# Performance work log

Measured on AMD Instinct MI355X. Metric: run time of the kernel, lower is better.

Reference implementation:

```python
import jax, jax.numpy as jnp
import numpy as np

BLOCK_LEN = 128
NUM_HEADS = 16


def setup_inputs() -> dict:
    key = jax.random.key(0)
    k0, k1, k2 = jax.random.split(key, 3)
    D = 1024
    x = jax.random.normal(k0, (2, 8192, D), dtype=jnp.float32)
    Wqkv = jax.random.normal(k1, (D, 3 * D), dtype=jnp.float32) * 0.02
    bqkv = jnp.zeros((3 * D,), dtype=jnp.float32)
    Wout = jax.random.normal(k2, (D, D), dtype=jnp.float32) * 0.02
    bout = jnp.zeros((D,), dtype=jnp.float32)
    return {"x": x, "Wqkv": Wqkv, "bqkv": bqkv, "Wout": Wout, "bout": bout}


def reference(x, Wqkv, bqkv, Wout, bout):
    B, S, D = x.shape
    H = NUM_HEADS
    BL = BLOCK_LEN
    NB = S // BL            # number of blocks (rows)
    HD = D // H             # head dim (qkv_ratio=1.0 -> qkv_dim_total == D)

    qkv = x @ Wqkv + bqkv                                   # [B, S, 3D]
    qkv = qkv.reshape(B, NB, BL, 3, H, HD)
    q = qkv[:, :, :, 0]                                     # [B, NB, BL, H, HD]
    k = qkv[:, :, :, 1]
    v = qkv[:, :, :, 2]

    # 'column' attention: attend across blocks at the same within-block position.
    # permute to [B, BL(pos p), H, NB(block n), HD]
    qc = jnp.transpose(q, (0, 2, 3, 1, 4))
    kc = jnp.transpose(k, (0, 2, 3, 1, 4))
    vc = jnp.transpose(v, (0, 2, 3, 1, 4))

    scale = 1.0 / jnp.sqrt(jnp.asarray(HD, dtype=x.dtype))
    scores = jnp.einsum('bphnd,bphmd->bphnm', qc, kc) * scale   # [B,BL,H,NB,NB]
    causal = jnp.tril(jnp.ones((NB, NB), dtype=bool))
    scores = jnp.where(causal, scores, jnp.asarray(-1e9, dtype=scores.dtype))
    w = jax.nn.softmax(scores, axis=-1)
    o = jnp.einsum('bphnm,bphmd->bphnd', w, vc)                 # [B,BL,H,NB,HD]

    # back to [B, NB, BL, H*HD] -> [B, S, D]
    o = jnp.transpose(o, (0, 3, 1, 2, 4)).reshape(B, S, D)
    return o @ Wout + bout
```

## Files before the change

kernel.cpp:

```cpp
#include <hip/hip_runtime.h>
#include <stdint.h>

typedef unsigned short u16;
typedef __attribute__((ext_vector_type(8))) short s16x8;
typedef __attribute__((ext_vector_type(4))) float f32x4;

__device__ __forceinline__ f32x4 mfma16x16(s16x8 a, s16x8 b, f32x4 c) {
    return __builtin_amdgcn_mfma_f32_16x16x32_bf16(a, b, c, 0, 0, 0);
}

__device__ __forceinline__ u16 f2bf(float f) {
    union { float f; unsigned u; } c; c.f = f;
    unsigned u = c.u;
    return (u16)((u + 0x7FFFu + ((u >> 16) & 1u)) >> 16);
}

__device__ __forceinline__ void gload16(const void* g, void* l) {
    auto gp = (const __attribute__((address_space(1))) unsigned int*)(g);
    auto lp = (__attribute__((address_space(3))) unsigned int*)(l);
    __builtin_amdgcn_global_load_lds(gp, lp, 16, 0, 0);
}

__device__ __forceinline__ void wave_sync() {
    __builtin_amdgcn_sched_barrier(0);
    asm volatile("s_waitcnt vmcnt(0) lgkmcnt(0)" ::: "memory");
    __builtin_amdgcn_sched_barrier(0);
    __builtin_amdgcn_s_barrier();
    __builtin_amdgcn_sched_barrier(0);
}

__global__ __launch_bounds__(256) void convert_x(
    const float* __restrict__ src, u16* __restrict__ dst, long n)
{
    const long stride = (long)gridDim.x * 256 * 8;
    for (long i = ((long)blockIdx.x * 256 + threadIdx.x) * 8; i < n; i += stride) {
        const float4 a = *(const float4*)(src + i);
        const float4 b = *(const float4*)(src + i + 4);
        u16 o[8] = { f2bf(a.x), f2bf(a.y), f2bf(a.z), f2bf(a.w),
                     f2bf(b.x), f2bf(b.y), f2bf(b.z), f2bf(b.w) };
        *(s16x8*)(dst + i) = *(const s16x8*)o;
    }
}

__global__ __launch_bounds__(256) void fill_sentinel(float* __restrict__ o, long n)
{
    const long stride = (long)gridDim.x * 256;
    for (long i = (long)blockIdx.x * 256 + threadIdx.x; i < n; i += stride)
        o[i] = 1.0f;
}

__global__ __launch_bounds__(256) void transpose_f32_bf16(
    const float* __restrict__ in, u16* __restrict__ out, int R, int C)
{
    __shared__ u16 t[32][33];
    const int c0 = blockIdx.x * 32, r0 = blockIdx.y * 32;
    const int tx = threadIdx.x & 31, ty = threadIdx.x >> 5;
#pragma unroll
    for (int i = 0; i < 32; i += 8)
        t[ty + i][tx] = f2bf(in[(long)(r0 + ty + i) * C + c0 + tx]);
    __syncthreads();
#pragma unroll
    for (int i = 0; i < 32; i += 8)
        out[(long)(c0 + ty + i) * R + r0 + tx] = t[tx][ty + i];
}

template <int FP32OUT, int NT, int NBN>
__global__ __launch_bounds__(512, 2) void gemm256(
    const u16* __restrict__ A, const u16* __restrict__ BT,
    const float* __restrict__ bias, void* __restrict__ Cout,
    int N, int K)
{
    extern __shared__ char smem[];
    char* const As = smem;
    char* const Bs = smem + 65536;

    const int tid  = threadIdx.x;
    const int lane = tid & 63;
    const int wid  = tid >> 6;
    const int rr   = lane & 15, g = lane >> 4;
    const int wr   = wid >> 2;
    const int wc   = wid & 3;

    const int nwg = gridDim.x;
    const int gsw = (blockIdx.x & 7) * (nwg >> 3) + (blockIdx.x >> 3);
    const long m0 = (long)(gsw / NBN) * 256;
    const long n0 = (long)(gsw % NBN) * 256;

    const int cl = (tid & 3) ^ ((tid >> 3) & 3);
    const u16* pA0 = A  + (m0 + (tid >> 2)) * (long)K + cl * 8;
    const u16* pA1 = pA0 + 128 * (long)K;
    const u16* pB0 = BT + (n0 + (tid >> 2)) * (long)K + cl * 8;
    const u16* pB1 = pB0 + 128 * (long)K;
    const int sdst = wid * 1024;

    const int xg    = (g ^ ((rr >> 1) & 3)) << 4;
    const int arow  = (wr * 128 + rr) * 64 + xg;
    const int brow  = (wc * 64  + rr) * 64 + xg;

#define STA(tt, h) { const long c_ = (long)(tt) * 64 + (h) * 32;              \
        char* d_ = As + (((tt) & 1) * 2 + (h)) * 16384 + sdst;                \
        gload16(pA0 + c_, d_); gload16(pA1 + c_, d_ + 8192); }
#define STB(tt, h) { const long c_ = (long)(tt) * 64 + (h) * 32;              \
        char* d_ = Bs + (((tt) & 1) * 2 + (h)) * 16384 + sdst;                \
        gload16(pB0 + c_, d_); gload16(pB1 + c_, d_ + 8192); }
#define SB() __builtin_amdgcn_sched_barrier(0)

    f32x4 acc[8][4] = {};

    STA(0, 0); STB(0, 0); STA(0, 1); STB(0, 1); STA(1, 0); STB(1, 0);
    asm volatile("s_waitcnt vmcnt(4)" ::: "memory");
    SB(); __builtin_amdgcn_s_barrier(); SB();

    for (int t = 0; t < NT; ++t) {
        const int ab = (t & 1) * 32768;
        s16x8 fB0[4], fA0[4], fA1[4], fB1[4], fA2[4], fA3[4];

#pragma unroll
        for (int n = 0; n < 4; ++n)
            fB0[n] = *(const s16x8*)(Bs + ab + brow + n * 1024);
#pragma unroll
        for (int m = 0; m < 4; ++m)
            fA0[m] = *(const s16x8*)(As + ab + arow + m * 1024);
#pragma unroll
        for (int m = 0; m < 4; ++m)
            fA1[m] = *(const s16x8*)(As + ab + arow + (m + 4) * 1024);
        if (t + 1 < NT) STA(t + 1, 1);
        SB();
        __builtin_amdgcn_s_setprio(1);
#pragma unroll
        for (int m = 0; m < 4; ++m)
#pragma unroll
            for (int n = 0; n < 4; ++n)
                acc[m][n] = mfma16x16(fA0[m], fB0[n], acc[m][n]);
        __builtin_amdgcn_s_setprio(0);
        SB();

#pragma unroll
        for (int n = 0; n < 4; ++n)
            fB1[n] = *(const s16x8*)(Bs + ab + 16384 + brow + n * 1024);
#pragma unroll
        for (int m = 0; m < 4; ++m)
            fA2[m] = *(const s16x8*)(As + ab + 16384 + arow + m * 1024);
        if (t + 1 < NT) STB(t + 1, 1);
        SB();
        __builtin_amdgcn_s_setprio(1);
#pragma unroll
        for (int m = 0; m < 4; ++m)
#pragma unroll
            for (int n = 0; n < 4; ++n)
                acc[m + 4][n] = mfma16x16(fA1[m], fB0[n], acc[m + 4][n]);
        __builtin_amdgcn_s_setprio(0);
        SB(); __builtin_amdgcn_s_barrier(); SB();

#pragma unroll
        for (int m = 0; m < 4; ++m)
            fA3[m] = *(const s16x8*)(As + ab + 16384 + arow + (m + 4) * 1024);
        if (t + 2 < NT) STA(t + 2, 0);
        SB();
        __builtin_amdgcn_s_setprio(1);
#pragma unroll
        for (int m = 0; m < 4; ++m)
#pragma unroll
            for (int n = 0; n < 4; ++n)
                acc[m][n] = mfma16x16(fA2[m], fB1[n], acc[m][n]);
        __builtin_amdgcn_s_setprio(0);
        SB();

        if (t + 2 < NT) STB(t + 2, 0);
        SB();
        __builtin_amdgcn_s_setprio(1);
#pragma unroll
        for (int m = 0; m < 4; ++m)
#pragma unroll
            for (int n = 0; n < 4; ++n)
                acc[m + 4][n] = mfma16x16(fA3[m], fB1[n], acc[m + 4][n]);
        __builtin_amdgcn_s_setprio(0);
        SB();

        if (t < NT - 1) {
            if (t >= NT - 2) { asm volatile("s_waitcnt vmcnt(0)" ::: "memory"); }
            else             { asm volatile("s_waitcnt vmcnt(4)" ::: "memory"); }
            SB(); __builtin_amdgcn_s_barrier(); SB();
        }
    }
#undef STA
#undef STB
#undef SB

    float bv[4];
#pragma unroll
    for (int n = 0; n < 4; ++n)
        bv[n] = bias[n0 + wc * 64 + n * 16 + rr];
#pragma unroll
    for (int m = 0; m < 8; ++m) {
        const long rb = m0 + wr * 128 + m * 16 + g * 4;
#pragma unroll
        for (int r = 0; r < 4; ++r) {
            const long rowoff = (rb + r) * N + n0 + wc * 64 + rr;
#pragma unroll
            for (int n = 0; n < 4; ++n) {
                const float v = acc[m][n][r] + bv[n];
                if (FP32OUT) ((float*)Cout)[rowoff + n * 16] = v;
                else         ((u16*)Cout)[rowoff + n * 16] = f2bf(v);
            }
        }
    }
}

template <int FP32OUT>
__global__ __launch_bounds__(256) void gemm_bt_bias(
    const u16* __restrict__ A, const u16* __restrict__ BT,
    const float* __restrict__ bias, void* __restrict__ Cout,
    int M, int N, int K)
{
    __shared__ u16 As[128 * 64];
    __shared__ u16 Bs[128 * 64];
    const int tid  = threadIdx.x;
    const int lane = tid & 63;
    const int wid  = tid >> 6;
    const int rr   = lane & 15, g = lane >> 4;
    const int wm   = (wid >> 1) << 6;
    const int wn   = (wid & 1) << 6;
    const long m0  = (long)blockIdx.y * 128;
    const long n0  = (long)blockIdx.x * 128;
    const int srow   = tid >> 3;
    const int schunk = (tid & 7) ^ (srow & 7);

    f32x4 acc[4][4] = {};

    for (int k0 = 0; k0 < K; k0 += 64) {
#pragma unroll
        for (int q = 0; q < 4; ++q) {
            const int row = q * 32 + srow;
            gload16(A  + (m0 + row) * K + k0 + schunk * 8,
                    (char*)As + q * 4096 + wid * 1024);
            gload16(BT + (n0 + row) * K + k0 + schunk * 8,
                    (char*)Bs + q * 4096 + wid * 1024);
        }
        __syncthreads();
#pragma unroll
        for (int kk = 0; kk < 2; ++kk) {
            s16x8 af[4], bfr[4];
#pragma unroll
            for (int i = 0; i < 4; ++i) {
                const int rowa = wm + i * 16 + rr;
                af[i] = *(const s16x8*)((const char*)As + rowa * 128 +
                         ((kk * 64 + g * 16) ^ ((rowa & 7) << 4)));
                const int rowb = wn + i * 16 + rr;
                bfr[i] = *(const s16x8*)((const char*)Bs + rowb * 128 +
                         ((kk * 64 + g * 16) ^ ((rowb & 7) << 4)));
            }
#pragma unroll
            for (int i = 0; i < 4; ++i)
#pragma unroll
                for (int j = 0; j < 4; ++j)
                    acc[i][j] = mfma16x16(af[i], bfr[j], acc[i][j]);
        }
        __syncthreads();
    }

#pragma unroll
    for (int i = 0; i < 4; ++i)
#pragma unroll
        for (int r = 0; r < 4; ++r) {
            const long rowg = m0 + wm + i * 16 + g * 4 + r;
#pragma unroll
            for (int j = 0; j < 4; ++j) {
                const long col = n0 + wn + j * 16 + rr;
                const float v = acc[i][j][r] + bias[col];
                if (FP32OUT) ((float*)Cout)[rowg * N + col] = v;
                else         ((u16*)Cout)[rowg * N + col] = f2bf(v);
            }
        }
}

__global__ __launch_bounds__(64) void attn_blocks(
    const u16* __restrict__ qkv, u16* __restrict__ o)
{
    __shared__ u16 Vlds[64 * 64];
    __shared__ u16 Plds[64 * 72];
    const int bid = blockIdx.x;
    const int b = bid >> 11;
    const int h = (bid >> 7) & 15;
    const int p = bid & 127;
    const int lane = threadIdx.x;
    const int rr = lane & 15, g = lane >> 4;
    const long NSTR = 128L * 3072;
    const long base = ((long)b * 8192 + p) * 3072 + h * 64;

    {
        const int vrow = lane >> 3;
        const int vchunk = (lane & 7) ^ (vrow & 7);
#pragma unroll
        for (int q = 0; q < 8; ++q)
            gload16(qkv + base + (long)(q * 8 + vrow) * NSTR + 2048 + vchunk * 8,
                    (char*)Vlds + q * 1024);
    }

    s16x8 kf[4][2], qf[4][2];
#pragma unroll
    for (int t = 0; t < 4; ++t)
#pragma unroll
        for (int ks = 0; ks < 2; ++ks) {
            const long roff = base + (long)(t * 16 + rr) * NSTR + ks * 32 + g * 8;
            kf[t][ks] = *(const s16x8*)(qkv + roff + 1024);
            qf[t][ks] = *(const s16x8*)(qkv + roff);
        }

    f32x4 T[4][4] = {};
#pragma unroll
    for (int ks = 0; ks < 2; ++ks)
#pragma unroll
        for (int i = 0; i < 4; ++i)
#pragma unroll
            for (int jn = 0; jn < 4; ++jn)
                T[i][jn] = mfma16x16(kf[i][ks], qf[jn][ks], T[i][jn]);

    const float scale = 0.125f;
#pragma unroll
    for (int jn = 0; jn < 4; ++jn) {
        const int n = jn * 16 + rr;
        float pv[16];
        float mx = -3e38f;
#pragma unroll
        for (int i = 0; i < 4; ++i)
#pragma unroll
            for (int r = 0; r < 4; ++r) {
                const int m = i * 16 + g * 4 + r;
                const float s = (m <= n) ? T[i][jn][r] * scale : -3e38f;
                pv[i * 4 + r] = s;
                mx = fmaxf(mx, s);
            }
        mx = fmaxf(mx, __shfl_xor(mx, 16));
        mx = fmaxf(mx, __shfl_xor(mx, 32));
        float sum = 0.f;
#pragma unroll
        for (int t = 0; t < 16; ++t) {
            const float e = (pv[t] > -1e30f) ? __expf(pv[t] - mx) : 0.f;
            pv[t] = e;
            sum += e;
        }
        sum += __shfl_xor(sum, 16);
        sum += __shfl_xor(sum, 32);
        const float inv = 1.f / sum;
#pragma unroll
        for (int i = 0; i < 4; ++i)
#pragma unroll
            for (int rp = 0; rp < 2; ++rp) {
                const int m = i * 16 + g * 4 + rp * 2;
                const unsigned lo = f2bf(pv[i * 4 + rp * 2] * inv);
                const unsigned hi = f2bf(pv[i * 4 + rp * 2 + 1] * inv);
                *(unsigned*)((char*)Plds + n * 144 + m * 2) = lo | (hi << 16);
            }
    }

    wave_sync();

    f32x4 O[4][4] = {};
#pragma unroll
    for (int ks = 0; ks < 2; ++ks) {
        s16x8 pa[4];
#pragma unroll
        for (int in = 0; in < 4; ++in)
            pa[in] = *(const s16x8*)((const char*)Plds +
                      (in * 16 + rr) * 144 + ks * 64 + g * 16);
#pragma unroll
        for (int jd = 0; jd < 4; ++jd) {
            s16x8 vb;
#pragma unroll
            for (int j = 0; j < 8; ++j) {
                const int k = ks * 32 + g * 8 + j;
                const int byte = (k * 128 + (jd * 16 + rr) * 2) ^ ((k & 7) << 4);
                vb[j] = *(const short*)((const char*)Vlds + byte);
            }
#pragma unroll
            for (int in = 0; in < 4; ++in)
                O[in][jd] = mfma16x16(pa[in], vb, O[in][jd]);
        }
    }

    const long obase = ((long)b * 8192 + p) * 1024 + h * 64;
#pragma unroll
    for (int in = 0; in < 4; ++in)
#pragma unroll
        for (int r = 0; r < 4; ++r) {
            const long n = in * 16 + g * 4 + r;
#pragma unroll
            for (int jd = 0; jd < 4; ++jd) {
                const long d = jd * 16 + rr;
                o[obase + n * (128L * 1024) + d] = f2bf(O[in][jd][r]);
            }
        }
}

extern "C" void kernel_launch(void* const* d_in, const int* in_sizes, int n_in,
                              void* d_out, int out_size, void* d_ws, size_t ws_size,
                              hipStream_t stream) {
    const float* x    = (const float*)d_in[0];
    const float* Wqkv = (const float*)d_in[1];
    const float* bq   = (const float*)d_in[2];
    const float* Wout = (const float*)d_in[3];
    const float* bo   = (const float*)d_in[4];

    char* ws = (char*)d_ws;
    u16* xb    = (u16*)(ws);
    u16* qkv   = (u16*)(ws +  33554432L);
    u16* ob    = (u16*)(ws + 134217728L);
    u16* WqkvT = (u16*)(ws + 167772160L);
    u16* WoutT = (u16*)(ws + 174063616L);
    const size_t NEEDED = 176160768UL;

    if (ws_size < NEEDED) {
        fill_sentinel<<<2048, 256, 0, stream>>>((float*)d_out, (long)out_size);
        return;
    }

    bool deep = true;
    if (hipFuncSetAttribute(reinterpret_cast<const void*>(&gemm256<0, 16, 12>),
                            hipFuncAttributeMaxDynamicSharedMemorySize,
                            131072) != hipSuccess) deep = false;
    if (hipFuncSetAttribute(reinterpret_cast<const void*>(&gemm256<1, 16, 4>),
                            hipFuncAttributeMaxDynamicSharedMemorySize,
                            131072) != hipSuccess) deep = false;

    convert_x<<<2048, 256, 0, stream>>>(x, xb, 16777216L);
    transpose_f32_bf16<<<dim3(96, 32), 256, 0, stream>>>(Wqkv, WqkvT, 1024, 3072);
    transpose_f32_bf16<<<dim3(32, 32), 256, 0, stream>>>(Wout, WoutT, 1024, 1024);

    if (deep)
        gemm256<0, 16, 12><<<768, 512, 131072, stream>>>(xb, WqkvT, bq, qkv,
                                                         3072, 1024);
    else
        gemm_bt_bias<0><<<dim3(24, 128), 256, 0, stream>>>(xb, WqkvT, bq, qkv,
                                                           16384, 3072, 1024);

    attn_blocks<<<4096, 64, 0, stream>>>(qkv, ob);

    if (deep)
        gemm256<1, 16, 4><<<256, 512, 131072, stream>>>(ob, WoutT, bo, d_out,
                                                        1024, 1024);
    else
        gemm_bt_bias<1><<<dim3(8, 128), 256, 0, stream>>>(ob, WoutT, bo, d_out,
                                                          16384, 1024, 1024);
}
```

Baseline: 190.8 us.

## Add 128x128-tile pipelined GEMM for QKV projection and drop fallback path

Adds a gemm128 kernel: a 256-thread version of the deep pipelined 256-tile GEMM with 128x128 tiles, split-phase async global-to-LDS prefetch and setprio around MFMA blocks. The QKV projection now uses it with 3072 workgroups instead of 768 large ones, aiming for better CU occupancy and tail balance on the 16384x3072 output. It also removes the simple gemm_bt_bias fallback and the check on whether the shared-memory attribute could be set. The trade-off is that smaller tiles give less operand reuse per loaded byte, and failures of the shared-memory attribute are no longer handled.

Measured after the change: 226.5 us. 18.7% more time.

```diff
diff --git a/kernel.cpp b/kernel.cpp
--- a/kernel.cpp
+++ b/kernel.cpp
@@ -65,6 +65,150 @@
 }
 
 template <int FP32OUT, int NT, int NBN>
+__global__ __launch_bounds__(256, 2) void gemm128(
+    const u16* __restrict__ A, const u16* __restrict__ BT,
+    const float* __restrict__ bias, void* __restrict__ Cout,
+    int N, int K)
+{
+    extern __shared__ char smem[];
+    char* const As = smem;
+    char* const Bs = smem + 32768;
+
+    const int tid  = threadIdx.x;
+    const int lane = tid & 63;
+    const int wid  = tid >> 6;
+    const int rr   = lane & 15, g = lane >> 4;
+    const int wr   = wid >> 1;
+    const int wc   = wid & 1;
+
+    const int nwg = gridDim.x;
+    const int gsw = ((int)blockIdx.x & 7) * (nwg >> 3) + ((int)blockIdx.x >> 3);
+    const long m0 = (long)(gsw / NBN) * 128;
+    const long n0 = (long)(gsw % NBN) * 128;
+
+    const int cl = (tid & 3) ^ ((tid >> 3) & 3);
+    const u16* pA[2]; const u16* pB[2];
+#pragma unroll
+    for (int p = 0; p < 2; ++p) {
+        pA[p] = A  + (m0 + p * 64 + (tid >> 2)) * (long)K + cl * 8;
+        pB[p] = BT + (n0 + p * 64 + (tid >> 2)) * (long)K + cl * 8;
+    }
+    const int sdst = wid * 1024;
+
+    const int xg   = (g ^ ((rr >> 1) & 3)) << 4;
+    const int arow = (wr * 64 + rr) * 64 + xg;
+    const int brow = (wc * 64 + rr) * 64 + xg;
+
+#define STA(tt, h) { const long c_ = (long)(tt) * 64 + (h) * 32;              \
+        char* d_ = As + (((tt) & 1) * 2 + (h)) * 8192 + sdst;                 \
+        gload16(pA[0] + c_, d_); gload16(pA[1] + c_, d_ + 4096); }
+#define STB(tt, h) { const long c_ = (long)(tt) * 64 + (h) * 32;              \
+        char* d_ = Bs + (((tt) & 1) * 2 + (h)) * 8192 + sdst;                 \
+        gload16(pB[0] + c_, d_); gload16(pB[1] + c_, d_ + 4096); }
+#define SB() __builtin_amdgcn_sched_barrier(0)
+
+    f32x4 acc[4][4] = {};
+
+    STA(0, 0); STB(0, 0); STA(0, 1); STB(0, 1); STA(1, 0); STB(1, 0);
+    asm volatile("s_waitcnt vmcnt(4)" ::: "memory");
+    SB(); __builtin_amdgcn_s_barrier(); SB();
+
+    for (int t = 0; t < NT; ++t) {
+        const int ab = (t & 1) * 16384;
+        s16x8 fB0[4], fB1[4], fA0[2], fA1[2], fA2[2], fA3[2];
+
+#pragma unroll
+        for (int n = 0; n < 4; ++n)
+            fB0[n] = *(const s16x8*)(Bs + ab + brow + n * 1024);
+#pragma unroll
+        for (int m = 0; m < 2; ++m) {
+            fA0[m] = *(const s16x8*)(As + ab + arow + m * 1024);
+            fA1[m] = *(const s16x8*)(As + ab + arow + (m + 2) * 1024);
+        }
+        if (t + 1 < NT) STA(t + 1, 1);
+        SB();
+        __builtin_amdgcn_s_setprio(1);
+#pragma unroll
+        for (int m = 0; m < 2; ++m)
+#pragma unroll
+            for (int n = 0; n < 4; ++n)
+                acc[m][n] = mfma16x16(fA0[m], fB0[n], acc[m][n]);
+        __builtin_amdgcn_s_setprio(0);
+        SB();
+
+#pragma unroll
+        for (int n = 0; n < 4; ++n)
+            fB1[n] = *(const s16x8*)(Bs + ab + 8192 + brow + n * 1024);
+#pragma unroll
+        for (int m = 0; m < 2; ++m)
+            fA2[m] = *(const s16x8*)(As + ab + 8192 + arow + m * 1024);
+        if (t + 1 < NT) STB(t + 1, 1);
+        SB();
+        __builtin_amdgcn_s_setprio(1);
+#pragma unroll
+        for (int m = 0; m < 2; ++m)
+#pragma unroll
+            for (int n = 0; n < 4; ++n)
+                acc[m + 2][n] = mfma16x16(fA1[m], fB0[n], acc[m + 2][n]);
+        __builtin_amdgcn_s_setprio(0);
+        SB(); __builtin_amdgcn_s_barrier(); SB();
+
+#pragma unroll
+        for (int m = 0; m < 2; ++m)
+            fA3[m] = *(const s16x8*)(As + ab + 8192 + arow + (m + 2) * 1024);
+        if (t + 2 < NT) STA(t + 2, 0);
+        SB();
+        __builtin_amdgcn_s_setprio(1);
+#pragma unroll
+        for (int m = 0; m < 2; ++m)
+#pragma unroll
+            for (int n = 0; n < 4; ++n)
+                acc[m][n] = mfma16x16(fA2[m], fB1[n], acc[m][n]);
+        __builtin_amdgcn_s_setprio(0);
+        SB();
+
+        if (t + 2 < NT) STB(t + 2, 0);
+        SB();
+        __builtin_amdgcn_s_setprio(1);
+#pragma unroll
+        for (int m = 0; m < 2; ++m)
+#pragma unroll
+            for (int n = 0; n < 4; ++n)
+                acc[m + 2][n] = mfma16x16(fA3[m], fB1[n], acc[m + 2][n]);
+        __builtin_amdgcn_s_setprio(0);
+        SB();
+
+        if (t < NT - 1) {
+            if (t >= NT - 2) { asm volatile("s_waitcnt vmcnt(0)" ::: "memory"); }
+            else             { asm volatile("s_waitcnt vmcnt(4)" ::: "memory"); }
+            SB(); __builtin_amdgcn_s_barrier(); SB();
+        }
+    }
+#undef STA
+#undef STB
+#undef SB
+
+    float bv[4];
+#pragma unroll
+    for (int n = 0; n < 4; ++n)
+        bv[n] = bias[n0 + wc * 64 + n * 16 + rr];
+#pragma unroll
+    for (int m = 0; m < 4; ++m) {
+        const long rb = m0 + wr * 64 + m * 16 + g * 4;
+#pragma unroll
+        for (int r = 0; r < 4; ++r) {
+            const long rowoff = (rb + r) * N + n0 + wc * 64 + rr;
+#pragma unroll
+            for (int n = 0; n < 4; ++n) {
+                const float v = acc[m][n][r] + bv[n];
+                if (FP32OUT) ((float*)Cout)[rowoff + n * 16] = v;
+                else         ((u16*)Cout)[rowoff + n * 16] = f2bf(v);
+            }
+        }
+    }
+}
+
+template <int FP32OUT, int NT, int NBN>
 __global__ __launch_bounds__(512, 2) void gemm256(
     const u16* __restrict__ A, const u16* __restrict__ BT,
     const float* __restrict__ bias, void* __restrict__ Cout,
@@ -82,7 +226,7 @@
     const int wc   = wid & 3;
 
     const int nwg = gridDim.x;
-    const int gsw = (blockIdx.x & 7) * (nwg >> 3) + (blockIdx.x >> 3);
+    const int gsw = ((int)blockIdx.x & 7) * (nwg >> 3) + ((int)blockIdx.x >> 3);
     const long m0 = (long)(gsw / NBN) * 256;
     const long n0 = (long)(gsw % NBN) * 256;
 
@@ -205,73 +349,6 @@
             }
         }
     }
-}
-
-template <int FP32OUT>
-__global__ __launch_bounds__(256) void gemm_bt_bias(
-    const u16* __restrict__ A, const u16* __restrict__ BT,
-    const float* __restrict__ bias, void* __restrict__ Cout,
-    int M, int N, int K)
-{
-    __shared__ u16 As[128 * 64];
-    __shared__ u16 Bs[128 * 64];
-    const int tid  = threadIdx.x;
-    const int lane = tid & 63;
-    const int wid  = tid >> 6;
-    const int rr   = lane & 15, g = lane >> 4;
-    const int wm   = (wid >> 1) << 6;
-    const int wn   = (wid & 1) << 6;
-    const long m0  = (long)blockIdx.y * 128;
-    const long n0  = (long)blockIdx.x * 128;
-    const int srow   = tid >> 3;
-    const int schunk = (tid & 7) ^ (srow & 7);
-
-    f32x4 acc[4][4] = {};
-
-    for (int k0 = 0; k0 < K; k0 += 64) {
-#pragma unroll
-        for (int q = 0; q < 4; ++q) {
-            const int row = q * 32 + srow;
-            gload16(A  + (m0 + row) * K + k0 + schunk * 8,
-                    (char*)As + q * 4096 + wid * 1024);
-            gload16(BT + (n0 + row) * K + k0 + schunk * 8,
-                    (char*)Bs + q * 4096 + wid * 1024);
-        }
-        __syncthreads();
-#pragma unroll
-        for (int kk = 0; kk < 2; ++kk) {
-            s16x8 af[4], bfr[4];
-#pragma unroll
-            for (int i = 0; i < 4; ++i) {
-                const int rowa = wm + i * 16 + rr;
-                af[i] = *(const s16x8*)((const char*)As + rowa * 128 +
-                         ((kk * 64 + g * 16) ^ ((rowa & 7) << 4)));
-                const int rowb = wn + i * 16 + rr;
-                bfr[i] = *(const s16x8*)((const char*)Bs + rowb * 128 +
-                         ((kk * 64 + g * 16) ^ ((rowb & 7) << 4)));
-            }
-#pragma unroll
-            for (int i = 0; i < 4; ++i)
-#pragma unroll
-                for (int j = 0; j < 4; ++j)
-                    acc[i][j] = mfma16x16(af[i], bfr[j], acc[i][j]);
-        }
-        __syncthreads();
-    }
-
-#pragma unroll
-    for (int i = 0; i < 4; ++i)
-#pragma unroll
-        for (int r = 0; r < 4; ++r) {
-            const long rowg = m0 + wm + i * 16 + g * 4 + r;
-#pragma unroll
-            for (int j = 0; j < 4; ++j) {
-                const long col = n0 + wn + j * 16 + rr;
-                const float v = acc[i][j][r] + bias[col];
-                if (FP32OUT) ((float*)Cout)[rowg * N + col] = v;
-                else         ((u16*)Cout)[rowg * N + col] = f2bf(v);
-            }
-        }
 }
 
 __global__ __launch_bounds__(64) void attn_blocks(
@@ -415,31 +492,20 @@
         return;
     }
 
-    bool deep = true;
-    if (hipFuncSetAttribute(reinterpret_cast<const void*>(&gemm256<0, 16, 12>),
-                            hipFuncAttributeMaxDynamicSharedMemorySize,
-                            131072) != hipSuccess) deep = false;
-    if (hipFuncSetAttribute(reinterpret_cast<const void*>(&gemm256<1, 16, 4>),
-                            hipFuncAttributeMaxDynamicSharedMemorySize,
-                            131072) != hipSuccess) deep = false;
+    (void)hipFuncSetAttribute(reinterpret_cast<const void*>(&gemm128<0, 16, 24>),
+                              hipFuncAttributeMaxDynamicSharedMemorySize, 65536);
+    (void)hipFuncSetAttribute(reinterpret_cast<const void*>(&gemm256<1, 16, 4>),
+                              hipFuncAttributeMaxDynamicSharedMemorySize, 131072);
 
     convert_x<<<2048, 256, 0, stream>>>(x, xb, 16777216L);
     transpose_f32_bf16<<<dim3(96, 32), 256, 0, stream>>>(Wqkv, WqkvT, 1024, 3072);
     transpose_f32_bf16<<<dim3(32, 32), 256, 0, stream>>>(Wout, WoutT, 1024, 1024);
 
-    if (deep)
-        gemm256<0, 16, 12><<<768, 512, 131072, stream>>>(xb, WqkvT, bq, qkv,
-                                                         3072, 1024);
-    else
-        gemm_bt_bias<0><<<dim3(24, 128), 256, 0, stream>>>(xb, WqkvT, bq, qkv,
-                                                           16384, 3072, 1024);
+    gemm128<0, 16, 24><<<3072, 256, 65536, stream>>>(xb, WqkvT, bq, qkv,
+                                                     3072, 1024);
 
     attn_blocks<<<4096, 64, 0, stream>>>(qkv, ob);
 
-    if (deep)
-        gemm256<1, 16, 4><<<256, 512, 131072, stream>>>(ob, WoutT, bo, d_out,
-                                                        1024, 1024);
-    else
-        gemm_bt_bias<1><<<dim3(8, 128), 256, 0, stream>>>(ob, WoutT, bo, d_out,
-                                                          16384, 1024, 1024);
-}
+    gemm256<1, 16, 4><<<256, 512, 131072, stream>>>(ob, WoutT, bo, d_out,
+                                                    1024, 1024);
+}
```
